# Kernel tuning notes

Hardware: AMD Instinct MI355X
Metric: run time of the kernel (lower is better)

Reference implementation:

```python
import jax, jax.numpy as jnp
import numpy as np

H = 16  # n_heads
D = 1024  # embed_dim == input_dim
FF = 4 * D
EPS = 1e-5  # torch LayerNorm default


def layer_norm(x, g, b):
    m = x.mean(-1, keepdims=True)
    v = x.var(-1, keepdims=True)
    return (x - m) / jnp.sqrt(v + EPS) * g + b


def setup_inputs() -> dict:
    key = jax.random.key(0)
    ks = jax.random.split(key, 8)
    s = lambda k, sh: (jax.random.normal(k, sh, jnp.float32) * 0.02)
    return {
        "kq": jax.random.normal(ks[0], (4, 2048, 512), jnp.float32),
        "v": jax.random.normal(ks[1], (4, 2048, 512), jnp.float32),
        "Wk": s(ks[2], (D, D)), "bk": jnp.zeros((D,), jnp.float32),
        "Wq": s(ks[3], (D, D)), "bq": jnp.zeros((D,), jnp.float32),
        "Wv": s(ks[4], (D, D)), "bv": jnp.zeros((D,), jnp.float32),
        "W1": s(ks[5], (FF, D)), "b1": jnp.zeros((FF,), jnp.float32),
        "W2": s(ks[6], (D, FF)), "b2": jnp.zeros((D,), jnp.float32),
        "g1": jnp.ones((D,), jnp.float32), "be1": jnp.zeros((D,), jnp.float32),
        "g2": jnp.ones((D,), jnp.float32), "be2": jnp.zeros((D,), jnp.float32),
    }


def reference(kq, v, Wk, bk, Wq, bq, Wv, bv, W1, b1, W2, b2, g1, be1, g2, be2):
    X = jnp.concatenate([kq, v], axis=-1)  # [n, T, input_dim]
    n, T, _ = kq.shape

    def heads(y):  # [n, T, D] -> [n, H, T, hd]
        return y.reshape(n, T, H, -1).transpose(0, 2, 1, 3)

    K = heads(X @ Wk.T + bk)
    Q = heads(X @ Wq.T + bq)
    V = heads(X @ Wv.T + bv)

    # NOTE: source applies no 1/sqrt(head_dim) scaling
    scores = jnp.einsum('nhqd,nhkd->nhqk', Q, K)
    causal = jnp.tril(jnp.ones((T, T), bool))  # mask = -inf strictly above diagonal
    scores = jnp.where(causal, scores, -jnp.inf)
    A = jax.nn.softmax(scores, axis=-1)
    attn_out = jnp.einsum('nhqk,nhkd->nhqd', A, V)
    attn_out = attn_out.transpose(0, 2, 1, 3).reshape(n, T, -1)  # [n, T, D]

    Vflat = V.transpose(0, 2, 1, 3).reshape(n, T, -1)  # residual is V projection, per source
    h = layer_norm(Vflat + attn_out, g1, be1)
    ff = jax.nn.gelu(h @ W1.T + b1, approximate=False) @ W2.T + b2  # torch GELU default = exact erf
    return layer_norm(h + ff, g2, be2)
```

## Files before the change

### kernel.cpp

```cpp
#include <hip/hip_runtime.h>
#include <stdint.h>

#define SEQ 2048
#define DM  1024
#define NH  16
#define HD  64
#define FFD 4096
#define TOK 8192

typedef __bf16 bf16x8 __attribute__((ext_vector_type(8)));
typedef float  f32x4  __attribute__((ext_vector_type(4)));
typedef float  f32x16 __attribute__((ext_vector_type(16)));
typedef unsigned short u16x8 __attribute__((ext_vector_type(8)));
typedef unsigned short u16x4 __attribute__((ext_vector_type(4)));
typedef unsigned int   u32x4 __attribute__((ext_vector_type(4)));

__device__ __forceinline__ unsigned short f2bf(float f) {
  unsigned u = __builtin_bit_cast(unsigned, f);
  u += 0x7fffu + ((u >> 16) & 1u);
  return (unsigned short)(u >> 16);
}
__device__ __forceinline__ float bf2f(unsigned short h) {
  return __builtin_bit_cast(float, ((unsigned)h) << 16);
}
__device__ __forceinline__ f32x4 mfma16(bf16x8 a, bf16x8 b, f32x4 c) {
  return __builtin_amdgcn_mfma_f32_16x16x32_bf16(a, b, c, 0, 0, 0);
}
__device__ __forceinline__ f32x16 mfma32(bf16x8 a, bf16x8 b, f32x16 c) {
  return __builtin_amdgcn_mfma_f32_32x32x16_bf16(a, b, c, 0, 0, 0);
}
__device__ __forceinline__ unsigned cvtpk(float lo, float hi) {
  unsigned r;
  asm("v_cvt_pk_bf16_f32 %0, %1, %2" : "=v"(r) : "v"(lo), "v"(hi));
  return r;
}
__device__ __forceinline__ void gld_lds16(void* lds, const void* g) {
  __builtin_amdgcn_global_load_lds((__attribute__((address_space(1))) void*)g,
                                   (__attribute__((address_space(3))) void*)lds,
                                   16, 0, 0);
}

__global__ __launch_bounds__(256) void concat_cast(
    const float* __restrict__ kq, const float* __restrict__ v,
    unsigned short* __restrict__ X) {
  int i = (blockIdx.x * 256 + threadIdx.x) * 4;
  int tkn = i >> 10;
  int c = i & 1023;
  const float* s = (c < 512) ? (kq + (size_t)tkn * 512 + c)
                             : (v  + (size_t)tkn * 512 + (c - 512));
  f32x4 f = *(const f32x4*)s;
  u16x4 o = { f2bf(f[0]), f2bf(f[1]), f2bf(f[2]), f2bf(f[3]) };
  *(u16x4*)&X[i] = o;
}

__global__ __launch_bounds__(256) void cast_f2b(
    const float* __restrict__ src, unsigned short* __restrict__ dst, int n) {
  int i = (blockIdx.x * 256 + threadIdx.x) * 4;
  if (i >= n) return;
  f32x4 f = *(const f32x4*)&src[i];
  u16x4 o = { f2bf(f[0]), f2bf(f[1]), f2bf(f[2]), f2bf(f[3]) };
  *(u16x4*)&dst[i] = o;
}

template<int EPI>
__global__ __launch_bounds__(256, 3) void gemm_bt(
    const unsigned short* __restrict__ A, const unsigned short* __restrict__ B,
    const float* __restrict__ bias, void* __restrict__ Cout,
    int M, int N, int K) {
  __shared__ __align__(16) unsigned short As[128 * 32];
  __shared__ __align__(16) unsigned short Bs[128 * 32];
  const int tid = threadIdx.x;
  const int w = tid >> 6, l = tid & 63;
  const int lr = l & 15, lg = l >> 4;
  const int bm = blockIdx.x * 128, bn = blockIdx.y * 128;
  const int wm = (w >> 1) * 64, wn = (w & 1) * 64;
  const unsigned short* Ath = A + (size_t)(bm + (tid >> 2)) * K + (tid & 3) * 8;
  const unsigned short* Bth = B + (size_t)(bn + (tid >> 2)) * K + (tid & 3) * 8;
  unsigned short* AsW = As + w * 512;
  unsigned short* BsW = Bs + w * 512;
  const size_t rstep = (size_t)64 * K;
  f32x4 acc[4][4] = {};
  for (int k0 = 0; k0 < K; k0 += 32) {
    gld_lds16(AsW,        Ath + k0);
    gld_lds16(AsW + 2048, Ath + k0 + rstep);
    gld_lds16(BsW,        Bth + k0);
    gld_lds16(BsW + 2048, Bth + k0 + rstep);
    __syncthreads();
    bf16x8 af[4], bfr[4];
#pragma unroll
    for (int mt = 0; mt < 4; ++mt)
      af[mt] = *(const bf16x8*)&As[(wm + mt * 16 + lr) * 32 + lg * 8];
#pragma unroll
    for (int nt = 0; nt < 4; ++nt)
      bfr[nt] = *(const bf16x8*)&Bs[(wn + nt * 16 + lr) * 32 + lg * 8];
#pragma unroll
    for (int mt = 0; mt < 4; ++mt)
#pragma unroll
      for (int nt = 0; nt < 4; ++nt)
        acc[mt][nt] = mfma16(af[mt], bfr[nt], acc[mt][nt]);
    __syncthreads();
  }
#pragma unroll
  for (int mt = 0; mt < 4; ++mt) {
    int row0 = bm + wm + mt * 16 + lg * 4;
#pragma unroll
    for (int nt = 0; nt < 4; ++nt) {
      int col = bn + wn + nt * 16 + lr;
      float bcol = bias[col];
#pragma unroll
      for (int r = 0; r < 4; ++r) {
        float vv = acc[mt][nt][r] + bcol;
        int row = row0 + r;
        if (EPI == 2) vv = 0.5f * vv * (1.0f + erff(vv * 0.70710678118654752f));
        if (EPI == 0)
          ((float*)Cout)[(size_t)row * N + col] = vv;
        else if (EPI == 3) {
          int bb = row >> 11, t = row & 2047;
          int hh = col >> 6, dc = (col >> 4) & 3, dl = col & 15;
          ((unsigned short*)Cout)[((((size_t)(bb * 16 + hh) * 4 + dc) * 2048 + t) << 4) + dl] = f2bf(vv);
        } else
          ((unsigned short*)Cout)[(size_t)row * N + col] = f2bf(vv);
      }
    }
  }
}

__global__ __launch_bounds__(256) void vtrans_kernel(
    const unsigned short* __restrict__ Vb, unsigned short* __restrict__ VI) {
  __shared__ __align__(16) unsigned short T[64][72];
  const int tid = threadIdx.x;
  const int bh = blockIdx.x;
  const int b = bh >> 4, h = bh & 15;
  const int t0 = blockIdx.y * 64;
  const int m = tid & 7;
  const int rr = tid >> 3;
#pragma unroll
  for (int cc = 0; cc < 2; ++cc) {
    int tt = rr + cc * 32;
    u16x8 vv = *(const u16x8*)&Vb[((size_t)b * SEQ + t0 + tt) * DM + h * 64 + m * 8];
    *(u16x8*)&T[tt][(m ^ (tt >> 3)) * 8] = vv;
  }
  __syncthreads();
#pragma unroll
  for (int cc = 0; cc < 2; ++cc) {
    int d = rr + cc * 32;
    u16x8 ov;
#pragma unroll
    for (int jj = 0; jj < 8; ++jj) {
      int tt = m * 8 + jj;
      ov[jj] = T[tt][((d >> 3) ^ (tt >> 3)) * 8 + (d & 7)];
    }
    int kt = (t0 >> 4) + (m >> 1);
    *(u16x8*)&VI[(((size_t)bh * 128 + kt) * 64 + d) * 16 + (m & 1) * 8] = ov;
  }
}

__global__ __launch_bounds__(128, 4) void attn_kernel(
    const unsigned short* __restrict__ Q, const unsigned short* __restrict__ KI,
    const unsigned short* __restrict__ VI, unsigned short* __restrict__ O) {
  __shared__ __align__(16) unsigned short T[2][32 * 72];
  const int tid = threadIdx.x;
  const int w = tid >> 6, l = tid & 63;
  const int q32 = l & 31;
  const int g = l >> 5;
  const int x = blockIdx.x;
  const int bh = (x & 7) * 8 + (x >> 3);
  const int b = bh >> 4, h = bh & 15;
  const int u = 63 - (2 * (int)blockIdx.y + w);
  const size_t tok0 = (size_t)b * SEQ;
  const size_t hoff = (size_t)h * 64;
  const unsigned short* Kp = KI + (size_t)bh * 4 * SEQ * 16;
  const unsigned short* Vp = VI + (size_t)bh * 128 * 64 * 16;

  const int q0 = u * 32;
  const int qg = q0 + q32;

  bf16x8 qf[4];
#pragma unroll
  for (int ks = 0; ks < 4; ++ks)
    qf[ks] = *(const bf16x8*)&Q[(tok0 + qg) * DM + hoff + ks * 16 + g * 8];

  f32x16 ot0 = {}, ot1 = {};
  float m = -3.0e38f, lden = 0.f;

  bf16x8 kf[4], vf[4];
#pragma unroll
  for (int ks = 0; ks < 4; ++ks)
    kf[ks] = *(const bf16x8*)&Kp[((size_t)ks * SEQ + q32) * 16 + g * 8];
#pragma unroll
  for (int dt = 0; dt < 2; ++dt)
#pragma unroll
    for (int s = 0; s < 2; ++s)
      vf[dt * 2 + s] = *(const bf16x8*)&Vp[((size_t)s * 64 + dt * 32 + q32) * 16 + g * 8];

#pragma unroll 1
  for (int j = 0; j <= u; ++j) {
    f32x16 st = {};
    __builtin_amdgcn_s_setprio(1);
#pragma unroll
    for (int ks = 0; ks < 4; ++ks) st = mfma32(kf[ks], qf[ks], st);
    __builtin_amdgcn_s_setprio(0);
    const int jn = (j < u) ? j + 1 : u;
    bf16x8 kn[4], vn[4];
#pragma unroll
    for (int ks = 0; ks < 4; ++ks)
      kn[ks] = *(const bf16x8*)&Kp[((size_t)ks * SEQ + jn * 32 + q32) * 16 + g * 8];
#pragma unroll
    for (int dt = 0; dt < 2; ++dt)
#pragma unroll
      for (int s = 0; s < 2; ++s)
        vn[dt * 2 + s] = *(const bf16x8*)&Vp[(((size_t)jn * 2 + s) * 64 + dt * 32 + q32) * 16 + g * 8];
    if (j == u) {
#pragma unroll
      for (int r = 0; r < 16; ++r) {
        int kg = j * 32 + (r & 3) + 8 * (r >> 2) + 4 * g;
        if (kg > qg) st[r] = -3.0e38f;
      }
    }
    float x0 = fmaxf(st[0], st[1]),  x1 = fmaxf(st[2], st[3]);
    float x2 = fmaxf(st[4], st[5]),  x3 = fmaxf(st[6], st[7]);
    float x4 = fmaxf(st[8], st[9]),  x5 = fmaxf(st[10], st[11]);
    float x6 = fmaxf(st[12], st[13]), x7 = fmaxf(st[14], st[15]);
    x0 = fmaxf(x0, x1); x2 = fmaxf(x2, x3); x4 = fmaxf(x4, x5); x6 = fmaxf(x6, x7);
    x0 = fmaxf(x0, x2); x4 = fmaxf(x4, x6);
    float pmax = fmaxf(x0, x4);
    if (__any(pmax - m > 8.0f)) {
      float pp = fmaxf(pmax, __shfl_xor(pmax, 32, 64));
      float mnew = fmaxf(m, pp);
      float sc = __expf(m - mnew);
#pragma unroll
      for (int r = 0; r < 16; ++r) { ot0[r] *= sc; ot1[r] *= sc; }
      lden *= sc;
      m = mnew;
    }
    float p[16];
#pragma unroll
    for (int r = 0; r < 16; ++r) p[r] = __expf(st[r] - m);
    {
      float s0 = p[0] + p[1], s1 = p[2] + p[3], s2 = p[4] + p[5], s3 = p[6] + p[7];
      float s4 = p[8] + p[9], s5 = p[10] + p[11], s6 = p[12] + p[13], s7 = p[14] + p[15];
      s0 += s1; s2 += s3; s4 += s5; s6 += s7;
      s0 += s2; s4 += s6;
      lden += s0 + s4;
    }
    unsigned c0 = cvtpk(p[0], p[1]),   c1 = cvtpk(p[2], p[3]);
    unsigned c2 = cvtpk(p[4], p[5]),   c3 = cvtpk(p[6], p[7]);
    unsigned c4 = cvtpk(p[8], p[9]),   c5 = cvtpk(p[10], p[11]);
    unsigned c6 = cvtpk(p[12], p[13]), c7 = cvtpk(p[14], p[15]);
    unsigned y0 = __shfl_xor(c0, 32, 64), y1 = __shfl_xor(c1, 32, 64);
    unsigned y2 = __shfl_xor(c2, 32, 64), y3 = __shfl_xor(c3, 32, 64);
    unsigned y4 = __shfl_xor(c4, 32, 64), y5 = __shfl_xor(c5, 32, 64);
    unsigned y6 = __shfl_xor(c6, 32, 64), y7 = __shfl_xor(c7, 32, 64);
    u32x4 f0 = { g ? y2 : c0, g ? y3 : c1, g ? c2 : y0, g ? c3 : y1 };
    u32x4 f1 = { g ? y6 : c4, g ? y7 : c5, g ? c6 : y4, g ? c7 : y5 };
    bf16x8 pb0 = __builtin_bit_cast(bf16x8, f0);
    bf16x8 pb1 = __builtin_bit_cast(bf16x8, f1);
    __builtin_amdgcn_s_setprio(1);
    ot0 = mfma32(vf[0], pb0, ot0);
    ot0 = mfma32(vf[1], pb1, ot0);
    ot1 = mfma32(vf[2], pb0, ot1);
    ot1 = mfma32(vf[3], pb1, ot1);
    __builtin_amdgcn_s_setprio(0);
#pragma unroll
    for (int ks = 0; ks < 4; ++ks) kf[ks] = kn[ks];
#pragma unroll
    for (int q = 0; q < 4; ++q) vf[q] = vn[q];
  }
  lden += __shfl_xor(lden, 32, 64);
  float inv = 1.0f / lden;
#pragma unroll
  for (int r = 0; r < 16; ++r) {
    int d = (r & 3) + 8 * (r >> 2) + 4 * g;
    T[w][q32 * 72 + d]      = f2bf(ot0[r] * inv);
    T[w][q32 * 72 + 32 + d] = f2bf(ot1[r] * inv);
  }
#pragma unroll
  for (int j2 = 0; j2 < 4; ++j2) {
    int col = g * 32 + j2 * 8;
    u16x8 vv = *(const u16x8*)&T[w][q32 * 72 + col];
    *(u16x8*)&O[(tok0 + q0 + q32) * DM + hoff + col] = vv;
  }
}

template<int MODE>
__global__ __launch_bounds__(256) void ln_kernel(
    const unsigned short* __restrict__ Xa, const void* __restrict__ Xc,
    const float* __restrict__ g, const float* __restrict__ be,
    void* __restrict__ outp) {
  const int row = blockIdx.x, t = threadIdx.x;
  const size_t base = (size_t)row * DM + t * 4;
  float x[4];
  u16x4 a = *(const u16x4*)&Xa[base];
  if (MODE == 0) {
    u16x4 c = *(const u16x4*)&((const unsigned short*)Xc)[base];
#pragma unroll
    for (int i = 0; i < 4; ++i) x[i] = bf2f(a[i]) + bf2f(c[i]);
  } else {
    f32x4 c = *(const f32x4*)&((const float*)Xc)[base];
#pragma unroll
    for (int i = 0; i < 4; ++i) x[i] = bf2f(a[i]) + c[i];
  }
  float s = x[0] + x[1] + x[2] + x[3];
  float ss = x[0] * x[0] + x[1] * x[1] + x[2] * x[2] + x[3] * x[3];
#pragma unroll
  for (int m = 1; m < 64; m <<= 1) {
    s  += __shfl_xor(s, m, 64);
    ss += __shfl_xor(ss, m, 64);
  }
  __shared__ float red[8];
  const int w = t >> 6;
  if ((t & 63) == 0) { red[w * 2] = s; red[w * 2 + 1] = ss; }
  __syncthreads();
  s  = red[0] + red[2] + red[4] + red[6];
  ss = red[1] + red[3] + red[5] + red[7];
  const float mean = s * (1.0f / DM);
  const float var = ss * (1.0f / DM) - mean * mean;
  const float rstd = rsqrtf(var + 1e-5f);
  if (MODE == 0) {
    u16x4 o;
#pragma unroll
    for (int i = 0; i < 4; ++i) {
      int cx = t * 4 + i;
      o[i] = f2bf((x[i] - mean) * rstd * g[cx] + be[cx]);
    }
    *(u16x4*)&((unsigned short*)outp)[base] = o;
  } else {
    f32x4 o;
#pragma unroll
    for (int i = 0; i < 4; ++i) {
      int cx = t * 4 + i;
      o[i] = (x[i] - mean) * rstd * g[cx] + be[cx];
    }
    *(f32x4*)&((float*)outp)[base] = o;
  }
}

extern "C" void kernel_launch(void* const* d_in, const int* in_sizes, int n_in,
                              void* d_out, int out_size, void* d_ws, size_t ws_size,
                              hipStream_t stream) {
  (void)in_sizes; (void)n_in; (void)out_size; (void)ws_size;
  const float* kq  = (const float*)d_in[0];
  const float* v   = (const float*)d_in[1];
  const float* Wk  = (const float*)d_in[2];
  const float* bk  = (const float*)d_in[3];
  const float* Wq  = (const float*)d_in[4];
  const float* bq  = (const float*)d_in[5];
  const float* Wv  = (const float*)d_in[6];
  const float* bv  = (const float*)d_in[7];
  const float* W1  = (const float*)d_in[8];
  const float* b1  = (const float*)d_in[9];
  const float* W2  = (const float*)d_in[10];
  const float* b2  = (const float*)d_in[11];
  const float* g1  = (const float*)d_in[12];
  const float* be1 = (const float*)d_in[13];
  const float* g2  = (const float*)d_in[14];
  const float* be2 = (const float*)d_in[15];
  float* out = (float*)d_out;
  uint8_t* ws = (uint8_t*)d_ws;

  unsigned short* Xb  = (unsigned short*)(ws + 0);
  unsigned short* Wkb = (unsigned short*)(ws + 16777216);
  unsigned short* Wqb = (unsigned short*)(ws + 18874368);
  unsigned short* Wvb = (unsigned short*)(ws + 20971520);
  unsigned short* Qb  = (unsigned short*)(ws + 23068672);
  unsigned short* Kb  = (unsigned short*)(ws + 39845888);
  unsigned short* Ab  = (unsigned short*)(ws + 56623104);
  unsigned short* F1b = (unsigned short*)(ws + 0);
  unsigned short* W1b = (unsigned short*)(ws + 73400320);
  unsigned short* W2b = (unsigned short*)(ws + 81788928);
  unsigned short* Vb  = (unsigned short*)(ws + 90177536);
  unsigned short* Hb  = (unsigned short*)(ws + 106954752);
  float*          F2f = (float*)(ws + 123731968);
  unsigned short* VIg = (unsigned short*)(ws + 123731968);

  concat_cast<<<TOK * DM / 1024, 256, 0, stream>>>(kq, v, Xb);
  cast_f2b<<<1024, 256, 0, stream>>>(Wk, Wkb, DM * DM);
  cast_f2b<<<1024, 256, 0, stream>>>(Wq, Wqb, DM * DM);
  cast_f2b<<<1024, 256, 0, stream>>>(Wv, Wvb, DM * DM);
  cast_f2b<<<4096, 256, 0, stream>>>(W1, W1b, FFD * DM);
  cast_f2b<<<4096, 256, 0, stream>>>(W2, W2b, DM * FFD);

  gemm_bt<3><<<dim3(64, 8), 256, 0, stream>>>(Xb, Wkb, bk, Kb, TOK, DM, DM);
  gemm_bt<1><<<dim3(64, 8), 256, 0, stream>>>(Xb, Wqb, bq, Qb, TOK, DM, DM);
  gemm_bt<1><<<dim3(64, 8), 256, 0, stream>>>(Xb, Wvb, bv, Vb, TOK, DM, DM);

  vtrans_kernel<<<dim3(64, 32), 256, 0, stream>>>(Vb, VIg);
  attn_kernel<<<dim3(64, 32), 128, 0, stream>>>(Qb, Kb, VIg, Ab);

  ln_kernel<0><<<TOK, 256, 0, stream>>>(Vb, Ab, g1, be1, Hb);

  gemm_bt<2><<<dim3(64, 32), 256, 0, stream>>>(Hb, W1b, b1, F1b, TOK, FFD, DM);
  gemm_bt<0><<<dim3(64, 8), 256, 0, stream>>>(F1b, W2b, b2, F2f, TOK, DM, FFD);

  ln_kernel<1><<<TOK, 256, 0, stream>>>(Hb, F2f, g2, be2, out);
}
```

Baseline: 404.5 us.

## Replace GEMM with 256-wide double-buffered swizzled tile kernel

Replaces the 128x128 single-buffered GEMM with a 512-thread kernel using 128x256 or 256x256 tiles, a K step of 64, double-buffered LDS with XOR-swizzled layout, prefetch interleaved with MFMA quarters, setprio, and a block-index remap for L2 locality. The aim is more reuse per loaded tile, fewer bank conflicts, and overlap of global loads with compute. Dynamic LDS of 96-128 KB limits occupancy, and the FFN1 launch needs large shared memory to be allowed.

```diff
diff --git a/kernel.cpp b/kernel.cpp
--- a/kernel.cpp
+++ b/kernel.cpp
@@ -62,54 +62,112 @@
   *(u16x4*)&dst[i] = o;
 }
 
-template<int EPI>
-__global__ __launch_bounds__(256, 3) void gemm_bt(
+template<int BM, int EPI>
+__global__ __launch_bounds__(512, 2) void gemm256(
     const unsigned short* __restrict__ A, const unsigned short* __restrict__ B,
     const float* __restrict__ bias, void* __restrict__ Cout,
     int M, int N, int K) {
-  __shared__ __align__(16) unsigned short As[128 * 32];
-  __shared__ __align__(16) unsigned short Bs[128 * 32];
+  constexpr int MF = BM / 32;
+  constexpr int NA = BM / 64;
+  constexpr int MQ = MF / 2;
+  extern __shared__ __align__(16) unsigned short lds[];
+  unsigned short* Asm0 = lds;
+  unsigned short* Bsm0 = lds + 2 * BM * 64;
   const int tid = threadIdx.x;
-  const int w = tid >> 6, l = tid & 63;
-  const int lr = l & 15, lg = l >> 4;
-  const int bm = blockIdx.x * 128, bn = blockIdx.y * 128;
-  const int wm = (w >> 1) * 64, wn = (w & 1) * 64;
-  const unsigned short* Ath = A + (size_t)(bm + (tid >> 2)) * K + (tid & 3) * 8;
-  const unsigned short* Bth = B + (size_t)(bn + (tid >> 2)) * K + (tid & 3) * 8;
-  unsigned short* AsW = As + w * 512;
-  unsigned short* BsW = Bs + w * 512;
-  const size_t rstep = (size_t)64 * K;
-  f32x4 acc[4][4] = {};
-  for (int k0 = 0; k0 < K; k0 += 32) {
-    gld_lds16(AsW,        Ath + k0);
-    gld_lds16(AsW + 2048, Ath + k0 + rstep);
-    gld_lds16(BsW,        Bth + k0);
-    gld_lds16(BsW + 2048, Bth + k0 + rstep);
-    __syncthreads();
-    bf16x8 af[4], bfr[4];
-#pragma unroll
-    for (int mt = 0; mt < 4; ++mt)
-      af[mt] = *(const bf16x8*)&As[(wm + mt * 16 + lr) * 32 + lg * 8];
-#pragma unroll
-    for (int nt = 0; nt < 4; ++nt)
-      bfr[nt] = *(const bf16x8*)&Bs[(wn + nt * 16 + lr) * 32 + lg * 8];
-#pragma unroll
-    for (int mt = 0; mt < 4; ++mt)
-#pragma unroll
-      for (int nt = 0; nt < 4; ++nt)
-        acc[mt][nt] = mfma16(af[mt], bfr[nt], acc[mt][nt]);
-    __syncthreads();
-  }
-#pragma unroll
-  for (int mt = 0; mt < 4; ++mt) {
-    int row0 = bm + wm + mt * 16 + lg * 4;
-#pragma unroll
-    for (int nt = 0; nt < 4; ++nt) {
-      int col = bn + wn + nt * 16 + lr;
+  const int w = tid >> 6, l = tid & 63, lr = l & 15, lg = l >> 4;
+  const int wm = w >> 2, wn = w & 3;
+  const int nbm = M / BM;
+  const int cpx = gridDim.x >> 3;
+  const int bid = blockIdx.x;
+  const int sw = (bid & 7) * cpx + (bid >> 3);
+  const int bm = (sw % nbm) * BM;
+  const int bn = (sw / nbm) * 256;
+  const int NT = K >> 6;
+  const int srow = tid >> 3;
+  const int sc8  = tid & 7;
+
+  f32x4 acc[MF][4] = {};
+
+  auto stageA = [&](int kt, int bb) {
+    unsigned short* dst = Asm0 + bb * BM * 64;
+#pragma unroll
+    for (int i = 0; i < NA; ++i) {
+      int row = i * 64 + srow;
+      gld_lds16(dst + (i * 512 + w * 64) * 8,
+                &A[(size_t)(bm + row) * K + kt * 64 + ((sc8 ^ (row & 7)) << 3)]);
+    }
+  };
+  auto stageB = [&](int kt, int bb) {
+    unsigned short* dst = Bsm0 + bb * 256 * 64;
+#pragma unroll
+    for (int i = 0; i < 4; ++i) {
+      int row = i * 64 + srow;
+      gld_lds16(dst + (i * 512 + w * 64) * 8,
+                &B[(size_t)(bn + row) * K + kt * 64 + ((sc8 ^ (row & 7)) << 3)]);
+    }
+  };
+
+  stageA(0, 0);
+  stageB(0, 0);
+  __syncthreads();
+
+  for (int t = 0; t < NT; ++t) {
+    const int cur = t & 1;
+    const bool pre = (t + 1 < NT);
+    const unsigned short* As = Asm0 + cur * BM * 64;
+    const unsigned short* Bs = Bsm0 + cur * 256 * 64;
+#pragma unroll
+    for (int q = 0; q < 4; ++q) {
+      bf16x8 av[MQ][2], bv[2][2];
+#pragma unroll
+      for (int fr = 0; fr < MQ; ++fr)
+#pragma unroll
+        for (int kk = 0; kk < 2; ++kk) {
+          int row = wm * (BM / 2) + ((q >> 1) * MQ + fr) * 16 + lr;
+          int c8 = (kk * 4 + lg) ^ (row & 7);
+          av[fr][kk] = *(const bf16x8*)&As[row * 64 + c8 * 8];
+        }
+#pragma unroll
+      for (int fn = 0; fn < 2; ++fn)
+#pragma unroll
+        for (int kk = 0; kk < 2; ++kk) {
+          int row = wn * 64 + ((q & 1) * 2 + fn) * 16 + lr;
+          int c8 = (kk * 4 + lg) ^ (row & 7);
+          bv[fn][kk] = *(const bf16x8*)&Bs[row * 64 + c8 * 8];
+        }
+      if (q == 0 && pre) {
+        stageA(t + 1, cur ^ 1);
+        if (BM == 128) stageB(t + 1, cur ^ 1);
+      }
+      if (BM == 256 && q == 1 && pre) stageB(t + 1, cur ^ 1);
+      if (q == 3 && pre) asm volatile("s_waitcnt vmcnt(0)" ::: "memory");
+      __builtin_amdgcn_s_barrier();
+      asm volatile("s_waitcnt lgkmcnt(0)" ::: "memory");
+      __builtin_amdgcn_sched_barrier(0);
+      __builtin_amdgcn_s_setprio(1);
+#pragma unroll
+      for (int fr = 0; fr < MQ; ++fr)
+#pragma unroll
+        for (int fn = 0; fn < 2; ++fn)
+#pragma unroll
+          for (int kk = 0; kk < 2; ++kk)
+            acc[(q >> 1) * MQ + fr][(q & 1) * 2 + fn] =
+                mfma16(av[fr][kk], bv[fn][kk],
+                       acc[(q >> 1) * MQ + fr][(q & 1) * 2 + fn]);
+      __builtin_amdgcn_s_setprio(0);
+      __builtin_amdgcn_s_barrier();
+    }
+  }
+#pragma unroll
+  for (int mf = 0; mf < MF; ++mf) {
+    int row0 = bm + wm * (BM / 2) + mf * 16 + lg * 4;
+#pragma unroll
+    for (int nf = 0; nf < 4; ++nf) {
+      int col = bn + wn * 64 + nf * 16 + lr;
       float bcol = bias[col];
 #pragma unroll
       for (int r = 0; r < 4; ++r) {
-        float vv = acc[mt][nt][r] + bcol;
+        float vv = acc[mf][nf][r] + bcol;
         int row = row0 + r;
         if (EPI == 2) vv = 0.5f * vv * (1.0f + erff(vv * 0.70710678118654752f));
         if (EPI == 0)
@@ -380,17 +438,17 @@
   cast_f2b<<<4096, 256, 0, stream>>>(W1, W1b, FFD * DM);
   cast_f2b<<<4096, 256, 0, stream>>>(W2, W2b, DM * FFD);
 
-  gemm_bt<3><<<dim3(64, 8), 256, 0, stream>>>(Xb, Wkb, bk, Kb, TOK, DM, DM);
-  gemm_bt<1><<<dim3(64, 8), 256, 0, stream>>>(Xb, Wqb, bq, Qb, TOK, DM, DM);
-  gemm_bt<1><<<dim3(64, 8), 256, 0, stream>>>(Xb, Wvb, bv, Vb, TOK, DM, DM);
+  gemm256<128, 3><<<256, 512, 98304, stream>>>(Xb, Wkb, bk, Kb, TOK, DM, DM);
+  gemm256<128, 1><<<256, 512, 98304, stream>>>(Xb, Wqb, bq, Qb, TOK, DM, DM);
+  gemm256<128, 1><<<256, 512, 98304, stream>>>(Xb, Wvb, bv, Vb, TOK, DM, DM);
 
   vtrans_kernel<<<dim3(64, 32), 256, 0, stream>>>(Vb, VIg);
   attn_kernel<<<dim3(64, 32), 128, 0, stream>>>(Qb, Kb, VIg, Ab);
 
   ln_kernel<0><<<TOK, 256, 0, stream>>>(Vb, Ab, g1, be1, Hb);
 
-  gemm_bt<2><<<dim3(64, 32), 256, 0, stream>>>(Hb, W1b, b1, F1b, TOK, FFD, DM);
-  gemm_bt<0><<<dim3(64, 8), 256, 0, stream>>>(F1b, W2b, b2, F2f, TOK, DM, FFD);
+  gemm256<256, 2><<<512, 512, 131072, stream>>>(Hb, W1b, b1, F1b, TOK, FFD, DM);
+  gemm256<128, 0><<<256, 512, 98304, stream>>>(F1b, W2b, b2, F2f, TOK, DM, FFD);
 
   ln_kernel<1><<<TOK, 256, 0, stream>>>(Hb, F2f, g2, be2, out);
 }
```

New measurement: 419.7 us. 3.8% more time.
